# Kernel tuning notes

Measured on AMD Instinct MI355X. Metric: run time of the kernel, lower is better.

## Reference

```python
import jax, jax.numpy as jnp
import numpy as np

D = 128      # d_model
ED = 256     # d_inner = 2*d_model
N = 16       # d_state
DT = 8       # dt_rank = ceil(d_model/16)
K = 4        # d_conv
NL = 2       # n_layers
NC = 2       # n_classes
EPS = 1e-5


def setup_inputs() -> dict:
    key = jax.random.key(0)
    ks = jax.random.split(key, 16)
    L, IN = 12000, 1024
    s = 0.02
    inp = {}
    inp['x'] = jax.random.normal(ks[0], (1, L, IN), jnp.float32)
    inp['coords'] = jax.random.uniform(ks[1], (L, 2), jnp.float32)
    inp['fc1_w'] = jax.random.normal(ks[2], (IN, D), jnp.float32) * s
    inp['fc1_b'] = jnp.zeros((D,), jnp.float32)
    inp['rms_w'] = jnp.ones((NL, D), jnp.float32)
    inp['inproj_w'] = jax.random.normal(ks[3], (NL, D, 2 * ED), jnp.float32) * s
    inp['conv_w'] = jax.random.normal(ks[4], (NL, ED, K), jnp.float32) * s
    inp['conv_b'] = jnp.zeros((NL, ED), jnp.float32)
    inp['xproj_w'] = jax.random.normal(ks[5], (NL, ED, DT + 2 * N), jnp.float32) * s
    inp['dt_w'] = jax.random.normal(ks[6], (NL, DT, ED), jnp.float32) * s
    inp['dt_b'] = jax.random.normal(ks[7], (NL, ED), jnp.float32) * 0.1
    inp['A_log'] = jnp.log(jnp.broadcast_to(jnp.arange(1, N + 1, dtype=jnp.float32), (NL, ED, N)))
    inp['D_p'] = jnp.ones((NL, ED), jnp.float32)
    inp['outproj_w'] = jax.random.normal(ks[8], (NL, ED, D), jnp.float32) * s
    inp['ln_w'] = jnp.ones((D,), jnp.float32)
    inp['ln_b'] = jnp.zeros((D,), jnp.float32)
    inp['att_w1'] = jax.random.normal(ks[9], (D, 128), jnp.float32) * s
    inp['att_b1'] = jnp.zeros((128,), jnp.float32)
    inp['att_w2'] = jax.random.normal(ks[10], (128, 1), jnp.float32) * s
    inp['att_b2'] = jnp.zeros((1,), jnp.float32)
    inp['cls_w'] = jax.random.normal(ks[11], (D, NC), jnp.float32) * s
    inp['cls_b'] = jnp.zeros((NC,), jnp.float32)
    return inp


def _rmsnorm(x, w):
    return x * jax.lax.rsqrt(jnp.mean(x * x, axis=-1, keepdims=True) + EPS) * w


def _layernorm(x, w, b):
    m = jnp.mean(x, axis=-1, keepdims=True)
    v = jnp.mean((x - m) ** 2, axis=-1, keepdims=True)
    return (x - m) * jax.lax.rsqrt(v + EPS) * w + b


def _causal_conv(xb, w, b):
    # xb: [B,L,ED], w: [ED,K] depthwise causal conv
    xpad = jnp.pad(xb, ((0, 0), (K - 1, 0), (0, 0)))
    kern = w.T[:, None, :]  # [K,1,ED]
    out = jax.lax.conv_general_dilated(
        xpad, kern, window_strides=(1,), padding='VALID',
        feature_group_count=ED, dimension_numbers=('NWC', 'WIO', 'NWC'))
    return out + b


def _mamba_block(h, ipw, cw, cb, xpw, dtw, dtb, alog, dp, opw):
    # h: [B,L,D]
    xz = h @ ipw                                  # [B,L,2*ED]
    xb, z = xz[..., :ED], xz[..., ED:]
    xc = jax.nn.silu(_causal_conv(xb, cw, cb))    # [B,L,ED]
    dbl = xc @ xpw                                # [B,L,DT+2N]
    dlt, Bm, Cm = dbl[..., :DT], dbl[..., DT:DT + N], dbl[..., DT + N:]
    delta = jax.nn.softplus(dlt @ dtw + dtb)      # [B,L,ED]
    A = -jnp.exp(alog)                            # [ED,N]
    dA = jnp.exp(delta[..., None] * A)            # [B,L,ED,N]
    dBx = (delta * xc)[..., None] * Bm[:, :, None, :]

    def step(hs, inp):
        da, dbx, c = inp
        hs = da * hs + dbx                        # [B,ED,N]
        y = jnp.einsum('ben,bn->be', hs, c)
        return hs, y

    h0 = jnp.zeros((dA.shape[0], ED, N), dA.dtype)
    xs = (dA.transpose(1, 0, 2, 3), dBx.transpose(1, 0, 2, 3), Cm.transpose(1, 0, 2))
    _, ys = jax.lax.scan(step, h0, xs)            # [L,B,ED]
    y = ys.transpose(1, 0, 2) + dp * xc
    y = y * jax.nn.silu(z)
    return y @ opw                                # [B,L,D]


def reference(x, coords, fc1_w, fc1_b, rms_w, inproj_w, conv_w, conv_b, xproj_w,
              dt_w, dt_b, A_log, D_p, outproj_w, ln_w, ln_b,
              att_w1, att_b1, att_w2, att_b2, cls_w, cls_b):
    h = jax.nn.gelu(x @ fc1_w + fc1_b, approximate=False)
    for i in range(NL):
        h = h + _mamba_block(_rmsnorm(h, rms_w[i]), inproj_w[i], conv_w[i], conv_b[i],
                             xproj_w[i], dt_w[i], dt_b[i], A_log[i], D_p[i], outproj_w[i])
    h = _layernorm(h, ln_w, ln_b)
    A = jnp.tanh(h @ att_w1 + att_b1) @ att_w2 + att_b2   # [1,L,1]
    A = jax.nn.softmax(A.transpose(0, 2, 1), axis=-1)     # [1,1,L]
    pooled = jnp.einsum('bol,bld->bod', A, h)[0]          # [1,D]
    logits = pooled @ cls_w + cls_b                       # [1,NC]
    Y_prob = jax.nn.softmax(logits, axis=1)
    Y_hat = jnp.argmax(logits, axis=1)
    return (logits, Y_prob, Y_hat)
```

## Files before the change

### kernel.cpp

```cpp
#include <hip/hip_runtime.h>

#define LQ 12000
#define IN_D 1024
#define DM 128
#define EDM 256
#define NS 16
#define CCH 480
#define SCH 25
#define GN 32
#define GSZ 15

typedef __bf16 v8bf __attribute__((ext_vector_type(8)));
typedef __bf16 v4bf __attribute__((ext_vector_type(4)));
typedef float v4f __attribute__((ext_vector_type(4)));

__device__ __forceinline__ float wave_sum64(float v) {
#pragma unroll
  for (int o = 32; o > 0; o >>= 1) v += __shfl_xor(v, o);
  return v;
}
__device__ __forceinline__ float wave_max64(float v) {
#pragma unroll
  for (int o = 32; o > 0; o >>= 1) v = fmaxf(v, __shfl_xor(v, o));
  return v;
}

__device__ __forceinline__ void stage16(const __bf16* g, __bf16* l) {
#if __has_builtin(__builtin_amdgcn_global_load_lds)
  __builtin_amdgcn_global_load_lds(
      (const __attribute__((address_space(1))) unsigned int*)g,
      (__attribute__((address_space(3))) unsigned int*)l, 16, 0, 0);
#else
  *(float4*)l = *(const float4*)g;
#endif
}

template <int ACT, bool BIAS, bool ACCUM>
__global__ __launch_bounds__(256) void mgemm_k(const __bf16* __restrict__ A,
                                               const __bf16* __restrict__ Bt,
                                               const float* __restrict__ bias,
                                               float* __restrict__ C, int M,
                                               int K, int Cs, int Nv) {
  __shared__ __bf16 As[64 * 32];
  __shared__ __bf16 Bs[64 * 32];
  const int tid = threadIdx.x;
  const int lane = tid & 63, wid = tid >> 6;
  const int wr = wid >> 1, wc = wid & 1;
  const int row0 = blockIdx.y * 64, col0 = blockIdx.x * 64;
  const int frow = lane & 15, fk8 = (lane >> 4) * 8;
  const int srow = tid >> 2, skseg = (tid & 3) * 8;
  int garow = row0 + srow;
  if (garow >= M) garow = M - 1;
  const __bf16* gA = A + (size_t)garow * K + skseg;
  const __bf16* gB = Bt + (size_t)(col0 + srow) * K + skseg;
  __bf16* lA = As + tid * 8;
  __bf16* lB = Bs + tid * 8;
  v4f acc[2][2] = {};
  for (int kt = 0; kt < K; kt += 32) {
    stage16(gA + kt, lA);
    stage16(gB + kt, lB);
    __syncthreads();
    v8bf av[2], bv[2];
#pragma unroll
    for (int i = 0; i < 2; ++i)
      av[i] = *(const v8bf*)(As + (wr * 32 + i * 16 + frow) * 32 + fk8);
#pragma unroll
    for (int j = 0; j < 2; ++j)
      bv[j] = *(const v8bf*)(Bs + (wc * 32 + j * 16 + frow) * 32 + fk8);
#pragma unroll
    for (int i = 0; i < 2; ++i)
#pragma unroll
      for (int j = 0; j < 2; ++j)
        acc[i][j] =
            __builtin_amdgcn_mfma_f32_16x16x32_bf16(av[i], bv[j], acc[i][j], 0, 0, 0);
    __syncthreads();
  }
#pragma unroll
  for (int i = 0; i < 2; ++i) {
#pragma unroll
    for (int j = 0; j < 2; ++j) {
      int cc = col0 + wc * 32 + j * 16 + (lane & 15);
#pragma unroll
      for (int r = 0; r < 4; ++r) {
        int rr = row0 + wr * 32 + i * 16 + (lane >> 4) * 4 + r;
        if (rr < M && cc < Nv) {
          float v = acc[i][j][r];
          if (BIAS) v += bias[cc];
          if (ACT == 1) v = 0.5f * v * (1.f + erff(v * 0.70710678118654752f));
          if (ACT == 2) v = tanhf(v);
          float* cp = C + (size_t)rr * Cs + cc;
          if (ACCUM)
            *cp += v;
          else
            *cp = v;
        }
      }
    }
  }
}

__global__ __launch_bounds__(256) void castw_k(const float* __restrict__ fc1w,
                                               const float* __restrict__ ipw,
                                               const float* __restrict__ xpw,
                                               const float* __restrict__ opw,
                                               const float* __restrict__ a1w,
                                               __bf16* __restrict__ wp) {
  int idx = blockIdx.x * 256 + threadIdx.x;
  const float* src;
  int K, N, o, base;
  if (idx < 131072) {
    base = 0; o = idx; src = fc1w; K = 1024; N = 128;
  } else if (idx < 262144) {
    int t = idx - 131072; int s = t >> 16; o = t & 65535;
    src = ipw + (size_t)s * 65536; K = 128; N = 512; base = 131072 + (s << 16);
  } else if (idx < 327680) {
    int t = idx - 262144; int s = t >> 15; o = t & 32767;
    src = xpw + (size_t)s * 10240; K = 256; N = 40; base = 262144 + (s << 15);
  } else if (idx < 393216) {
    int t = idx - 327680; int s = t >> 15; o = t & 32767;
    src = opw + (size_t)s * 32768; K = 256; N = 128; base = 327680 + (s << 15);
  } else {
    base = 393216; o = idx - 393216; src = a1w; K = 128; N = 128;
  }
  int n = o / K, k = o - n * K;
  float v = (n < N) ? src[(size_t)k * N + n] : 0.f;
  wp[base + o] = (__bf16)v;
}

__global__ __launch_bounds__(256) void castx_k(const float* __restrict__ in,
                                               __bf16* __restrict__ out) {
  int i = blockIdx.x * 256 + threadIdx.x;
  float4 v = ((const float4*)in)[i];
  v4bf w = {(__bf16)v.x, (__bf16)v.y, (__bf16)v.z, (__bf16)v.w};
  ((v4bf*)out)[i] = w;
}

__global__ __launch_bounds__(256) void rmsnorm_k(const float* __restrict__ h,
                                                 const float* __restrict__ w,
                                                 __bf16* __restrict__ o) {
  int lane = threadIdx.x & 63;
  int t = blockIdx.x * 4 + (threadIdx.x >> 6);
  const float* row = h + (size_t)t * DM;
  float x0 = row[lane], x1 = row[lane + 64];
  float ss = wave_sum64(x0 * x0 + x1 * x1);
  float r = 1.f / sqrtf(ss * (1.f / DM) + 1e-5f);
  o[(size_t)t * DM + lane] = (__bf16)(x0 * r * w[lane]);
  o[(size_t)t * DM + lane + 64] = (__bf16)(x1 * r * w[lane + 64]);
}

__global__ __launch_bounds__(256) void layernorm_k(const float* __restrict__ h,
                                                   const float* __restrict__ w,
                                                   const float* __restrict__ b,
                                                   float* __restrict__ o,
                                                   __bf16* __restrict__ ob) {
  int lane = threadIdx.x & 63;
  int t = blockIdx.x * 4 + (threadIdx.x >> 6);
  const float* row = h + (size_t)t * DM;
  float x0 = row[lane], x1 = row[lane + 64];
  float s = wave_sum64(x0 + x1);
  float ss = wave_sum64(x0 * x0 + x1 * x1);
  float m = s * (1.f / DM);
  float var = ss * (1.f / DM) - m * m;
  float r = 1.f / sqrtf(var + 1e-5f);
  float y0 = (x0 - m) * r * w[lane] + b[lane];
  float y1 = (x1 - m) * r * w[lane + 64] + b[lane + 64];
  o[(size_t)t * DM + lane] = y0;
  o[(size_t)t * DM + lane + 64] = y1;
  ob[(size_t)t * DM + lane] = (__bf16)y0;
  ob[(size_t)t * DM + lane + 64] = (__bf16)y1;
}

__global__ __launch_bounds__(256) void conv_silu_k(const float* __restrict__ xz,
                                                   const float* __restrict__ cw,
                                                   const float* __restrict__ cb,
                                                   float* __restrict__ xc,
                                                   __bf16* __restrict__ xcb) {
  int idx = blockIdx.x * 256 + threadIdx.x;
  int e = idx & (EDM - 1);
  int t = idx >> 8;
  float acc = cb[e];
  const float* wp = cw + e * 4;
#pragma unroll
  for (int j = 0; j < 4; ++j) {
    int ts = t - 3 + j;
    if (ts >= 0) acc = fmaf(xz[(size_t)ts * 512 + e], wp[j], acc);
  }
  float v = __fdividef(acc, 1.f + __expf(-acc));
  xc[idx] = v;
  xcb[idx] = (__bf16)v;
}

__global__ __launch_bounds__(256) void dt_k(const float* __restrict__ dbl,
                                            const float* __restrict__ dtw,
                                            const float* __restrict__ dtb,
                                            float* __restrict__ delta) {
  int idx = blockIdx.x * 256 + threadIdx.x;
  int e = idx & 255;
  int t = idx >> 8;
  const float* dl = dbl + (size_t)t * 40;
  float acc = dtb[e];
#pragma unroll
  for (int k = 0; k < 8; ++k) acc = fmaf(dl[k], dtw[k * 256 + e], acc);
  delta[idx] = fmaxf(acc, 0.f) + log1pf(expf(-fabsf(acc)));
}


__global__ __launch_bounds__(256) void scan1_k(const float* __restrict__ delta,
                                               const float* __restrict__ xc,
                                               const float* __restrict__ dbl,
                                               float* __restrict__ Dsum,
                                               float* __restrict__ Bacc) {
  int e = threadIdx.x;
  int c = blockIdx.x;
  int t0 = c * SCH;
  float h[NS];
#pragma unroll
  for (int n = 0; n < NS; ++n) h[n] = 0.f;
  float ds = 0.f;
  const float* dp = delta + (size_t)t0 * EDM + e;
  const float* xp = xc + (size_t)t0 * EDM + e;
  const float* bp = dbl + (size_t)t0 * 40 + 8;
  for (int s = 0; s < SCH; ++s) {
    float d = dp[s * EDM];
    float xcv = xp[s * EDM];
    float q = __expf(-d);
    float dx = d * xcv;
    ds += d;
    const float* B = bp + s * 40;
    float pw = q;
#pragma unroll
    for (int n = 0; n < NS; ++n) {
      h[n] = fmaf(pw, h[n], dx * B[n]);
      pw *= q;
    }
  }
  Dsum[c * EDM + e] = ds;
  float4* bq = (float4*)(Bacc + (size_t)c * 4096 + e * NS);
  bq[0] = make_float4(h[0], h[1], h[2], h[3]);
  bq[1] = make_float4(h[4], h[5], h[6], h[7]);
  bq[2] = make_float4(h[8], h[9], h[10], h[11]);
  bq[3] = make_float4(h[12], h[13], h[14], h[15]);
}

__global__ __launch_bounds__(256) void scan2a_k(const float* __restrict__ alog,
                                                const float* __restrict__ Dsum,
                                                const float* __restrict__ Bacc,
                                                float* __restrict__ Gs,
                                                float* __restrict__ Gb) {
  int b = blockIdx.x;
  int g = b >> 4;
  int ch = ((b & 15) << 8) + threadIdx.x;
  int e = ch >> 4;
  float Aen = -expf(alog[ch]);
  float hh = 0.f, ds = 0.f;
#pragma unroll
  for (int j = 0; j < GSZ; ++j) {
    int c = g * GSZ + j;
    float dsv = Dsum[c * EDM + e];
    ds += dsv;
    hh = fmaf(__expf(Aen * dsv), hh, Bacc[(size_t)c * 4096 + ch]);
  }
  Gs[g * 4096 + ch] = ds;
  Gb[g * 4096 + ch] = hh;
}

__global__ __launch_bounds__(256) void scan2b_k(const float* __restrict__ alog,
                                                const float* __restrict__ Gs,
                                                const float* __restrict__ Gb,
                                                float* __restrict__ Gc) {
  int ch = blockIdx.x * 256 + threadIdx.x;
  float Aen = -expf(alog[ch]);
  float gs[GN], gb[GN];
#pragma unroll
  for (int g = 0; g < GN; ++g) {
    gs[g] = Gs[g * 4096 + ch];
    gb[g] = Gb[g * 4096 + ch];
  }
  float carry = 0.f;
#pragma unroll
  for (int g = 0; g < GN; ++g) {
    Gc[g * 4096 + ch] = carry;
    carry = fmaf(__expf(Aen * gs[g]), carry, gb[g]);
  }
}

__global__ __launch_bounds__(256) void scan2c_k(const float* __restrict__ alog,
                                                const float* __restrict__ Dsum,
                                                float* __restrict__ Bacc,
                                                const float* __restrict__ Gc) {
  int b = blockIdx.x;
  int g = b >> 4;
  int ch = ((b & 15) << 8) + threadIdx.x;
  int e = ch >> 4;
  float Aen = -expf(alog[ch]);
  float carry = Gc[g * 4096 + ch];
#pragma unroll
  for (int j = 0; j < GSZ; ++j) {
    int c = g * GSZ + j;
    float a = __expf(Aen * Dsum[c * EDM + e]);
    float old = Bacc[(size_t)c * 4096 + ch];
    Bacc[(size_t)c * 4096 + ch] = carry;
    carry = fmaf(a, carry, old);
  }
}

__global__ __launch_bounds__(256) void scan3_k(const float* __restrict__ delta,
                                               const float* __restrict__ xc,
                                               const float* __restrict__ dbl,
                                               const float* __restrict__ xz,
                                               const float* __restrict__ Bacc,
                                               const float* __restrict__ dpw,
                                               __bf16* __restrict__ yb) {
  int e = threadIdx.x;
  int c = blockIdx.x;
  int t0 = c * SCH;
  float h[NS];
  const float4* hq = (const float4*)(Bacc + (size_t)c * 4096 + e * NS);
  float4 h0 = hq[0], h1 = hq[1], h2 = hq[2], h3 = hq[3];
  h[0] = h0.x; h[1] = h0.y; h[2] = h0.z; h[3] = h0.w;
  h[4] = h1.x; h[5] = h1.y; h[6] = h1.z; h[7] = h1.w;
  h[8] = h2.x; h[9] = h2.y; h[10] = h2.z; h[11] = h2.w;
  h[12] = h3.x; h[13] = h3.y; h[14] = h3.z; h[15] = h3.w;
  float dpe = dpw[e];
  const float* dp = delta + (size_t)t0 * EDM + e;
  const float* xp = xc + (size_t)t0 * EDM + e;
  const float* bp = dbl + (size_t)t0 * 40 + 8;
  const float* zp = xz + (size_t)t0 * 512 + 256 + e;
  for (int s = 0; s < SCH; ++s) {
    float d = dp[s * EDM];
    float xcv = xp[s * EDM];
    float q = __expf(-d);
    float dx = d * xcv;
    const float* B = bp + s * 40;
    const float* Cc = B + NS;
    float v = 0.f;
    float pw = q;
#pragma unroll
    for (int n = 0; n < NS; ++n) {
      h[n] = fmaf(pw, h[n], dx * B[n]);
      v = fmaf(h[n], Cc[n], v);
      pw *= q;
    }
    float y = v + dpe * xcv;
    float z = zp[s * 512];
    y *= __fdividef(z, 1.f + __expf(-z));
    yb[(size_t)(t0 + s) * EDM + e] = (__bf16)y;
  }
}

__global__ __launch_bounds__(256) void att2_k(const float* __restrict__ t1,
                                              const float* __restrict__ w2,
                                              const float* __restrict__ b2,
                                              float* __restrict__ s) {
  int lane = threadIdx.x & 63;
  int t = blockIdx.x * 4 + (threadIdx.x >> 6);
  const float* row = t1 + (size_t)t * DM;
  float acc = fmaf(row[lane], w2[lane], row[lane + 64] * w2[lane + 64]);
  acc = wave_sum64(acc);
  if (lane == 0) s[t] = acc + b2[0];
}

__global__ __launch_bounds__(1024) void att_stats_k(const float* __restrict__ s,
                                                    float* __restrict__ stats) {
  __shared__ float red[16];
  int lane = threadIdx.x & 63, wid = threadIdx.x >> 6;
  float m = -1e30f;
  for (int i = threadIdx.x; i < LQ; i += 1024) m = fmaxf(m, s[i]);
  m = wave_max64(m);
  if (lane == 0) red[wid] = m;
  __syncthreads();
  if (threadIdx.x < 16) {
    float mm = red[threadIdx.x];
#pragma unroll
    for (int o = 8; o > 0; o >>= 1) mm = fmaxf(mm, __shfl_xor(mm, o));
    if (threadIdx.x == 0) red[0] = mm;
  }
  __syncthreads();
  float smax = red[0];
  __syncthreads();
  float sum = 0.f;
  for (int i = threadIdx.x; i < LQ; i += 1024) sum += expf(s[i] - smax);
  sum = wave_sum64(sum);
  if (lane == 0) red[wid] = sum;
  __syncthreads();
  if (threadIdx.x == 0) {
    float tot = 0.f;
    for (int i = 0; i < 16; ++i) tot += red[i];
    stats[0] = smax;
    stats[1] = tot;
  }
}

__global__ __launch_bounds__(128) void pooled_k(const float* __restrict__ s,
                                                const float* __restrict__ stats,
                                                const float* __restrict__ hn,
                                                float* __restrict__ pooled) {
  __shared__ float w[64];
  int t0 = blockIdx.x * 64;
  float smax = stats[0];
  if (threadIdx.x < 64) {
    int t = t0 + threadIdx.x;
    w[threadIdx.x] = (t < LQ) ? expf(s[t] - smax) : 0.f;
  }
  __syncthreads();
  int d = threadIdx.x;
  float acc = 0.f;
  int nmax = min(64, LQ - t0);
  for (int i = 0; i < nmax; ++i)
    acc = fmaf(w[i], hn[(size_t)(t0 + i) * DM + d], acc);
  atomicAdd(&pooled[d], acc);
}

__global__ __launch_bounds__(128) void final_k(const float* __restrict__ pooled,
                                               const float* __restrict__ stats,
                                               const float* __restrict__ cls_w,
                                               const float* __restrict__ cls_b,
                                               float* __restrict__ out) {
  __shared__ float r0[2], r1[2];
  int lane = threadIdx.x & 63, wid = threadIdx.x >> 6;
  float p = pooled[threadIdx.x] / stats[1];
  float v0 = p * cls_w[threadIdx.x * 2 + 0];
  float v1 = p * cls_w[threadIdx.x * 2 + 1];
  v0 = wave_sum64(v0);
  v1 = wave_sum64(v1);
  if (lane == 0) {
    r0[wid] = v0;
    r1[wid] = v1;
  }
  __syncthreads();
  if (threadIdx.x == 0) {
    float L0 = r0[0] + r0[1] + cls_b[0];
    float L1 = r1[0] + r1[1] + cls_b[1];
    float mx = fmaxf(L0, L1);
    float e0 = expf(L0 - mx), e1 = expf(L1 - mx);
    float inv = 1.f / (e0 + e1);
    out[0] = L0;
    out[1] = L1;
    out[2] = e0 * inv;
    out[3] = e1 * inv;
    out[4] = (L1 > L0) ? 1.f : 0.f;
  }
}

extern "C" void kernel_launch(void* const* d_in, const int* in_sizes, int n_in,
                              void* d_out, int out_size, void* d_ws,
                              size_t ws_size, hipStream_t stream) {
  const float* x = (const float*)d_in[0];
  const float* fc1_w = (const float*)d_in[2];
  const float* fc1_b = (const float*)d_in[3];
  const float* rms_w = (const float*)d_in[4];
  const float* inproj_w = (const float*)d_in[5];
  const float* conv_w = (const float*)d_in[6];
  const float* conv_b = (const float*)d_in[7];
  const float* xproj_w = (const float*)d_in[8];
  const float* dt_w = (const float*)d_in[9];
  const float* dt_b = (const float*)d_in[10];
  const float* A_log = (const float*)d_in[11];
  const float* D_p = (const float*)d_in[12];
  const float* outproj_w = (const float*)d_in[13];
  const float* ln_w = (const float*)d_in[14];
  const float* ln_b = (const float*)d_in[15];
  const float* att_w1 = (const float*)d_in[16];
  const float* att_b1 = (const float*)d_in[17];
  const float* att_w2 = (const float*)d_in[18];
  const float* att_b2 = (const float*)d_in[19];
  const float* cls_w = (const float*)d_in[20];
  const float* cls_b = (const float*)d_in[21];
  float* out = (float*)d_out;

  float* ws = (float*)d_ws;
  float* xz = ws;
  float* h = xz + 6144000;
  float* hn = h + 1536000;
  float* xc = hn + 1536000;
  float* dbl = xc + 3072000;
  float* del = dbl + 480000;
  float* Dsum = del + 3072000;
  float* Bacc = Dsum + 122880;
  float* Gs = Bacc + 1966080;
  float* Gb = Gs + 131072;
  float* Gc = Gb + 131072;
  float* pooled = Gc + 131072;
  float* stats = pooled + 128;
  __bf16* wp = (__bf16*)(stats + 16);
  __bf16* hnb = wp + 409600;
  __bf16* xcb = hnb + 1536000;
  __bf16* yb = xcb + 3072000;
  __bf16* xb = (__bf16*)xz;

  const __bf16* fc1T = wp;
  const __bf16* ipT[2] = {wp + 131072, wp + 196608};
  const __bf16* xpT[2] = {wp + 262144, wp + 294912};
  const __bf16* opT[2] = {wp + 327680, wp + 360448};
  const __bf16* a1T = wp + 393216;

  hipMemsetAsync(pooled, 0, 128 * sizeof(float), stream);

  dim3 b256(256);
  castw_k<<<1600, b256, 0, stream>>>(fc1_w, inproj_w, xproj_w, outproj_w,
                                     att_w1, wp);
  castx_k<<<12000, b256, 0, stream>>>(x, xb);
  mgemm_k<1, true, false><<<dim3(2, 188), b256, 0, stream>>>(
      xb, fc1T, fc1_b, h, LQ, 1024, 128, 128);

  for (int l = 0; l < 2; ++l) {
    const float* alog_l = A_log + l * 4096;
    rmsnorm_k<<<3000, b256, 0, stream>>>(h, rms_w + l * DM, hnb);
    mgemm_k<0, false, false><<<dim3(8, 188), b256, 0, stream>>>(
        hnb, ipT[l], nullptr, xz, LQ, 128, 512, 512);
    conv_silu_k<<<12000, b256, 0, stream>>>(xz, conv_w + l * EDM * 4,
                                            conv_b + l * EDM, xc, xcb);
    mgemm_k<0, false, false><<<dim3(1, 188), b256, 0, stream>>>(
        xcb, xpT[l], nullptr, dbl, LQ, 256, 40, 40);
    dt_k<<<12000, b256, 0, stream>>>(dbl, dt_w + l * 8 * EDM, dt_b + l * EDM,
                                     del);
    scan1_k<<<CCH, b256, 0, stream>>>(del, xc, dbl, Dsum, Bacc);
    scan2a_k<<<512, b256, 0, stream>>>(alog_l, Dsum, Bacc, Gs, Gb);
    scan2b_k<<<16, b256, 0, stream>>>(alog_l, Gs, Gb, Gc);
    scan2c_k<<<512, b256, 0, stream>>>(alog_l, Dsum, Bacc, Gc);
    scan3_k<<<CCH, b256, 0, stream>>>(del, xc, dbl, xz, Bacc, D_p + l * EDM,
                                      yb);
    mgemm_k<0, false, true><<<dim3(2, 188), b256, 0, stream>>>(
        yb, opT[l], nullptr, h, LQ, 256, 128, 128);
  }

  layernorm_k<<<3000, b256, 0, stream>>>(h, ln_w, ln_b, hn, hnb);
  mgemm_k<2, true, false><<<dim3(2, 188), b256, 0, stream>>>(
      hnb, a1T, att_b1, del, LQ, 128, 128, 128);
  att2_k<<<3000, b256, 0, stream>>>(del, att_w2, att_b2, dbl);
  att_stats_k<<<1, 1024, 0, stream>>>(dbl, stats);
  pooled_k<<<188, 128, 0, stream>>>(dbl, stats, hn, pooled);
  final_k<<<1, 128, 0, stream>>>(pooled, stats, cls_w, cls_b, out);
}
```

Baseline: 382.4 us.

## Fuse casts, dt projection, silu gate and attention head into neighboring kernels

Folds the fp32-to-bf16 cast of the input into the fc1 GEMM's A-tile staging, and recomputes the dt projection plus softplus inside both scan kernels instead of materialising delta. It also applies the z-gate silu in the in-proj GEMM epilogue and stores xz, xc and the layernorm output only as bf16. The attention tanh layer is fused with the w2 dot product through shuffles and atomics, which removes several kernels and a lot of fp32 intermediate traffic. In exchange there is more bf16 rounding in intermediates, redundant dt arithmetic in scan1 and scan3, and att_b2 is dropped (softmax is shift-invariant, so this is fine unless stats uses the raw scores).

```diff
diff --git a/kernel.cpp b/kernel.cpp
--- a/kernel.cpp
+++ b/kernel.cpp
@@ -11,7 +11,6 @@
 #define GSZ 15
 
 typedef __bf16 v8bf __attribute__((ext_vector_type(8)));
-typedef __bf16 v4bf __attribute__((ext_vector_type(4)));
 typedef float v4f __attribute__((ext_vector_type(4)));
 
 __device__ __forceinline__ float wave_sum64(float v) {
@@ -35,11 +34,10 @@
 #endif
 }
 
-template <int ACT, bool BIAS, bool ACCUM>
+template <int ACT, bool ACCUM, bool OBF>
 __global__ __launch_bounds__(256) void mgemm_k(const __bf16* __restrict__ A,
                                                const __bf16* __restrict__ Bt,
-                                               const float* __restrict__ bias,
-                                               float* __restrict__ C, int M,
+                                               void* __restrict__ Cv, int M,
                                                int K, int Cs, int Nv) {
   __shared__ __bf16 As[64 * 32];
   __shared__ __bf16 Bs[64 * 32];
@@ -71,30 +69,152 @@
     for (int i = 0; i < 2; ++i)
 #pragma unroll
       for (int j = 0; j < 2; ++j)
-        acc[i][j] =
-            __builtin_amdgcn_mfma_f32_16x16x32_bf16(av[i], bv[j], acc[i][j], 0, 0, 0);
+        acc[i][j] = __builtin_amdgcn_mfma_f32_16x16x32_bf16(av[i], bv[j],
+                                                            acc[i][j], 0, 0, 0);
     __syncthreads();
   }
 #pragma unroll
   for (int i = 0; i < 2; ++i) {
 #pragma unroll
     for (int j = 0; j < 2; ++j) {
-      int cc = col0 + wc * 32 + j * 16 + (lane & 15);
+      int cc = col0 + wc * 32 + j * 16 + frow;
 #pragma unroll
       for (int r = 0; r < 4; ++r) {
         int rr = row0 + wr * 32 + i * 16 + (lane >> 4) * 4 + r;
         if (rr < M && cc < Nv) {
           float v = acc[i][j][r];
-          if (BIAS) v += bias[cc];
-          if (ACT == 1) v = 0.5f * v * (1.f + erff(v * 0.70710678118654752f));
-          if (ACT == 2) v = tanhf(v);
-          float* cp = C + (size_t)rr * Cs + cc;
-          if (ACCUM)
-            *cp += v;
-          else
-            *cp = v;
+          if (ACT == 4 && cc >= 256) v = __fdividef(v, 1.f + __expf(-v));
+          if (OBF) {
+            ((__bf16*)Cv)[(size_t)rr * Cs + cc] = (__bf16)v;
+          } else {
+            float* cp = (float*)Cv + (size_t)rr * Cs + cc;
+            if (ACCUM)
+              *cp += v;
+            else
+              *cp = v;
+          }
         }
       }
+    }
+  }
+}
+
+__global__ __launch_bounds__(256) void fc1_k(const float* __restrict__ A,
+                                             const __bf16* __restrict__ Bt,
+                                             const float* __restrict__ bias,
+                                             float* __restrict__ C, int M,
+                                             int K) {
+  __shared__ __bf16 As[64 * 32];
+  __shared__ __bf16 Bs[64 * 32];
+  const int tid = threadIdx.x;
+  const int lane = tid & 63, wid = tid >> 6;
+  const int wr = wid >> 1, wc = wid & 1;
+  const int row0 = blockIdx.y * 64, col0 = blockIdx.x * 64;
+  const int frow = lane & 15, fk8 = (lane >> 4) * 8;
+  const int srow = tid >> 2, skseg = (tid & 3) * 8;
+  int garow = row0 + srow;
+  if (garow >= M) garow = M - 1;
+  const float* gA = A + (size_t)garow * K + skseg;
+  const __bf16* gB = Bt + (size_t)(col0 + srow) * K + skseg;
+  __bf16* lB = Bs + tid * 8;
+  v4f acc[2][2] = {};
+  for (int kt = 0; kt < K; kt += 32) {
+    float4 f0 = *(const float4*)(gA + kt);
+    float4 f1 = *(const float4*)(gA + kt + 4);
+    stage16(gB + kt, lB);
+    v8bf a8 = {(__bf16)f0.x, (__bf16)f0.y, (__bf16)f0.z, (__bf16)f0.w,
+               (__bf16)f1.x, (__bf16)f1.y, (__bf16)f1.z, (__bf16)f1.w};
+    *(v8bf*)(As + tid * 8) = a8;
+    __syncthreads();
+    v8bf av[2], bv[2];
+#pragma unroll
+    for (int i = 0; i < 2; ++i)
+      av[i] = *(const v8bf*)(As + (wr * 32 + i * 16 + frow) * 32 + fk8);
+#pragma unroll
+    for (int j = 0; j < 2; ++j)
+      bv[j] = *(const v8bf*)(Bs + (wc * 32 + j * 16 + frow) * 32 + fk8);
+#pragma unroll
+    for (int i = 0; i < 2; ++i)
+#pragma unroll
+      for (int j = 0; j < 2; ++j)
+        acc[i][j] = __builtin_amdgcn_mfma_f32_16x16x32_bf16(av[i], bv[j],
+                                                            acc[i][j], 0, 0, 0);
+    __syncthreads();
+  }
+#pragma unroll
+  for (int i = 0; i < 2; ++i) {
+#pragma unroll
+    for (int j = 0; j < 2; ++j) {
+      int cc = col0 + wc * 32 + j * 16 + frow;
+#pragma unroll
+      for (int r = 0; r < 4; ++r) {
+        int rr = row0 + wr * 32 + i * 16 + (lane >> 4) * 4 + r;
+        if (rr < M) {
+          float v = acc[i][j][r] + bias[cc];
+          v = 0.5f * v * (1.f + erff(v * 0.70710678118654752f));
+          C[(size_t)rr * DM + cc] = v;
+        }
+      }
+    }
+  }
+}
+
+__global__ __launch_bounds__(256) void att1_k(const __bf16* __restrict__ A,
+                                              const __bf16* __restrict__ Bt,
+                                              const float* __restrict__ b1,
+                                              const float* __restrict__ w2,
+                                              float* __restrict__ s, int M) {
+  __shared__ __bf16 As[64 * 32];
+  __shared__ __bf16 Bs[64 * 32];
+  const int tid = threadIdx.x;
+  const int lane = tid & 63, wid = tid >> 6;
+  const int wr = wid >> 1, wc = wid & 1;
+  const int row0 = blockIdx.y * 64, col0 = blockIdx.x * 64;
+  const int frow = lane & 15, fk8 = (lane >> 4) * 8;
+  const int srow = tid >> 2, skseg = (tid & 3) * 8;
+  const int K = 128;
+  int garow = row0 + srow;
+  if (garow >= M) garow = M - 1;
+  const __bf16* gA = A + (size_t)garow * K + skseg;
+  const __bf16* gB = Bt + (size_t)(col0 + srow) * K + skseg;
+  __bf16* lA = As + tid * 8;
+  __bf16* lB = Bs + tid * 8;
+  v4f acc[2][2] = {};
+  for (int kt = 0; kt < K; kt += 32) {
+    stage16(gA + kt, lA);
+    stage16(gB + kt, lB);
+    __syncthreads();
+    v8bf av[2], bv[2];
+#pragma unroll
+    for (int i = 0; i < 2; ++i)
+      av[i] = *(const v8bf*)(As + (wr * 32 + i * 16 + frow) * 32 + fk8);
+#pragma unroll
+    for (int j = 0; j < 2; ++j)
+      bv[j] = *(const v8bf*)(Bs + (wc * 32 + j * 16 + frow) * 32 + fk8);
+#pragma unroll
+    for (int i = 0; i < 2; ++i)
+#pragma unroll
+      for (int j = 0; j < 2; ++j)
+        acc[i][j] = __builtin_amdgcn_mfma_f32_16x16x32_bf16(av[i], bv[j],
+                                                            acc[i][j], 0, 0, 0);
+    __syncthreads();
+  }
+#pragma unroll
+  for (int i = 0; i < 2; ++i) {
+#pragma unroll
+    for (int r = 0; r < 4; ++r) {
+      float p = 0.f;
+#pragma unroll
+      for (int j = 0; j < 2; ++j) {
+        int cc = col0 + wc * 32 + j * 16 + frow;
+        p += tanhf(acc[i][j][r] + b1[cc]) * w2[cc];
+      }
+      p += __shfl_xor(p, 1);
+      p += __shfl_xor(p, 2);
+      p += __shfl_xor(p, 4);
+      p += __shfl_xor(p, 8);
+      int rr = row0 + wr * 32 + i * 16 + (lane >> 4) * 4 + r;
+      if (frow == 0 && rr < M) atomicAdd(&s[rr], p);
     }
   }
 }
@@ -127,14 +247,6 @@
   wp[base + o] = (__bf16)v;
 }
 
-__global__ __launch_bounds__(256) void castx_k(const float* __restrict__ in,
-                                               __bf16* __restrict__ out) {
-  int i = blockIdx.x * 256 + threadIdx.x;
-  float4 v = ((const float4*)in)[i];
-  v4bf w = {(__bf16)v.x, (__bf16)v.y, (__bf16)v.z, (__bf16)v.w};
-  ((v4bf*)out)[i] = w;
-}
-
 __global__ __launch_bounds__(256) void rmsnorm_k(const float* __restrict__ h,
                                                  const float* __restrict__ w,
                                                  __bf16* __restrict__ o) {
@@ -151,7 +263,6 @@
 __global__ __launch_bounds__(256) void layernorm_k(const float* __restrict__ h,
                                                    const float* __restrict__ w,
                                                    const float* __restrict__ b,
-                                                   float* __restrict__ o,
                                                    __bf16* __restrict__ ob) {
   int lane = threadIdx.x & 63;
   int t = blockIdx.x * 4 + (threadIdx.x >> 6);
@@ -162,18 +273,14 @@
   float m = s * (1.f / DM);
   float var = ss * (1.f / DM) - m * m;
   float r = 1.f / sqrtf(var + 1e-5f);
-  float y0 = (x0 - m) * r * w[lane] + b[lane];
-  float y1 = (x1 - m) * r * w[lane + 64] + b[lane + 64];
-  o[(size_t)t * DM + lane] = y0;
-  o[(size_t)t * DM + lane + 64] = y1;
-  ob[(size_t)t * DM + lane] = (__bf16)y0;
-  ob[(size_t)t * DM + lane + 64] = (__bf16)y1;
-}
-
-__global__ __launch_bounds__(256) void conv_silu_k(const float* __restrict__ xz,
+  ob[(size_t)t * DM + lane] = (__bf16)((x0 - m) * r * w[lane] + b[lane]);
+  ob[(size_t)t * DM + lane + 64] =
+      (__bf16)((x1 - m) * r * w[lane + 64] + b[lane + 64]);
+}
+
+__global__ __launch_bounds__(256) void conv_silu_k(const __bf16* __restrict__ xzb,
                                                    const float* __restrict__ cw,
                                                    const float* __restrict__ cb,
-                                                   float* __restrict__ xc,
                                                    __bf16* __restrict__ xcb) {
   int idx = blockIdx.x * 256 + threadIdx.x;
   int e = idx & (EDM - 1);
@@ -183,50 +290,47 @@
 #pragma unroll
   for (int j = 0; j < 4; ++j) {
     int ts = t - 3 + j;
-    if (ts >= 0) acc = fmaf(xz[(size_t)ts * 512 + e], wp[j], acc);
+    if (ts >= 0) acc = fmaf((float)xzb[(size_t)ts * 512 + e], wp[j], acc);
   }
   float v = __fdividef(acc, 1.f + __expf(-acc));
-  xc[idx] = v;
   xcb[idx] = (__bf16)v;
 }
 
-__global__ __launch_bounds__(256) void dt_k(const float* __restrict__ dbl,
-                                            const float* __restrict__ dtw,
-                                            const float* __restrict__ dtb,
-                                            float* __restrict__ delta) {
-  int idx = blockIdx.x * 256 + threadIdx.x;
-  int e = idx & 255;
-  int t = idx >> 8;
-  const float* dl = dbl + (size_t)t * 40;
-  float acc = dtb[e];
-#pragma unroll
-  for (int k = 0; k < 8; ++k) acc = fmaf(dl[k], dtw[k * 256 + e], acc);
-  delta[idx] = fmaxf(acc, 0.f) + log1pf(expf(-fabsf(acc)));
-}
-
-
-__global__ __launch_bounds__(256) void scan1_k(const float* __restrict__ delta,
-                                               const float* __restrict__ xc,
+
+__device__ __forceinline__ float softplus_f(float a) {
+  return fmaxf(a, 0.f) + log1pf(__expf(-fabsf(a)));
+}
+
+__global__ __launch_bounds__(256) void scan1_k(const __bf16* __restrict__ xcb,
                                                const float* __restrict__ dbl,
+                                               const float* __restrict__ dtw,
+                                               const float* __restrict__ dtb,
                                                float* __restrict__ Dsum,
                                                float* __restrict__ Bacc) {
   int e = threadIdx.x;
   int c = blockIdx.x;
   int t0 = c * SCH;
+  float w8[8];
+#pragma unroll
+  for (int k = 0; k < 8; ++k) w8[k] = dtw[k * 256 + e];
+  float dtbe = dtb[e];
   float h[NS];
 #pragma unroll
   for (int n = 0; n < NS; ++n) h[n] = 0.f;
   float ds = 0.f;
-  const float* dp = delta + (size_t)t0 * EDM + e;
-  const float* xp = xc + (size_t)t0 * EDM + e;
-  const float* bp = dbl + (size_t)t0 * 40 + 8;
+  const __bf16* xp = xcb + (size_t)t0 * EDM + e;
+  const float* rp = dbl + (size_t)t0 * 40;
   for (int s = 0; s < SCH; ++s) {
-    float d = dp[s * EDM];
-    float xcv = xp[s * EDM];
+    const float* row = rp + s * 40;
+    float a = dtbe;
+#pragma unroll
+    for (int k = 0; k < 8; ++k) a = fmaf(row[k], w8[k], a);
+    float d = softplus_f(a);
+    float xcv = (float)xp[s * EDM];
     float q = __expf(-d);
     float dx = d * xcv;
     ds += d;
-    const float* B = bp + s * 40;
+    const float* B = row + 8;
     float pw = q;
 #pragma unroll
     for (int n = 0; n < NS; ++n) {
@@ -304,16 +408,21 @@
   }
 }
 
-__global__ __launch_bounds__(256) void scan3_k(const float* __restrict__ delta,
-                                               const float* __restrict__ xc,
+__global__ __launch_bounds__(256) void scan3_k(const __bf16* __restrict__ xcb,
                                                const float* __restrict__ dbl,
-                                               const float* __restrict__ xz,
+                                               const float* __restrict__ dtw,
+                                               const float* __restrict__ dtb,
+                                               const __bf16* __restrict__ xzb,
                                                const float* __restrict__ Bacc,
                                                const float* __restrict__ dpw,
                                                __bf16* __restrict__ yb) {
   int e = threadIdx.x;
   int c = blockIdx.x;
   int t0 = c * SCH;
+  float w8[8];
+#pragma unroll
+  for (int k = 0; k < 8; ++k) w8[k] = dtw[k * 256 + e];
+  float dtbe = dtb[e];
   float h[NS];
   const float4* hq = (const float4*)(Bacc + (size_t)c * 4096 + e * NS);
   float4 h0 = hq[0], h1 = hq[1], h2 = hq[2], h3 = hq[3];
@@ -322,17 +431,20 @@
   h[8] = h2.x; h[9] = h2.y; h[10] = h2.z; h[11] = h2.w;
   h[12] = h3.x; h[13] = h3.y; h[14] = h3.z; h[15] = h3.w;
   float dpe = dpw[e];
-  const float* dp = delta + (size_t)t0 * EDM + e;
-  const float* xp = xc + (size_t)t0 * EDM + e;
-  const float* bp = dbl + (size_t)t0 * 40 + 8;
-  const float* zp = xz + (size_t)t0 * 512 + 256 + e;
+  const __bf16* xp = xcb + (size_t)t0 * EDM + e;
+  const float* rp = dbl + (size_t)t0 * 40;
+  const __bf16* zp = xzb + (size_t)t0 * 512 + 256 + e;
   for (int s = 0; s < SCH; ++s) {
-    float d = dp[s * EDM];
-    float xcv = xp[s * EDM];
+    const float* row = rp + s * 40;
+    float a = dtbe;
+#pragma unroll
+    for (int k = 0; k < 8; ++k) a = fmaf(row[k], w8[k], a);
+    float d = softplus_f(a);
+    float xcv = (float)xp[s * EDM];
     float q = __expf(-d);
     float dx = d * xcv;
-    const float* B = bp + s * 40;
-    const float* Cc = B + NS;
+    const float* B = row + 8;
+    const float* Cc = row + 24;
     float v = 0.f;
     float pw = q;
 #pragma unroll
@@ -341,23 +453,9 @@
       v = fmaf(h[n], Cc[n], v);
       pw *= q;
     }
-    float y = v + dpe * xcv;
-    float z = zp[s * 512];
-    y *= __fdividef(z, 1.f + __expf(-z));
+    float y = (v + dpe * xcv) * (float)zp[s * 512];
     yb[(size_t)(t0 + s) * EDM + e] = (__bf16)y;
   }
-}
-
-__global__ __launch_bounds__(256) void att2_k(const float* __restrict__ t1,
-                                              const float* __restrict__ w2,
-                                              const float* __restrict__ b2,
-                                              float* __restrict__ s) {
-  int lane = threadIdx.x & 63;
-  int t = blockIdx.x * 4 + (threadIdx.x >> 6);
-  const float* row = t1 + (size_t)t * DM;
-  float acc = fmaf(row[lane], w2[lane], row[lane + 64] * w2[lane + 64]);
-  acc = wave_sum64(acc);
-  if (lane == 0) s[t] = acc + b2[0];
 }
 
 __global__ __launch_bounds__(1024) void att_stats_k(const float* __restrict__ s,
@@ -393,7 +491,7 @@
 
 __global__ __launch_bounds__(128) void pooled_k(const float* __restrict__ s,
                                                 const float* __restrict__ stats,
-                                                const float* __restrict__ hn,
+                                                const __bf16* __restrict__ hnb,
                                                 float* __restrict__ pooled) {
   __shared__ float w[64];
   int t0 = blockIdx.x * 64;
@@ -407,7 +505,7 @@
   float acc = 0.f;
   int nmax = min(64, LQ - t0);
   for (int i = 0; i < nmax; ++i)
-    acc = fmaf(w[i], hn[(size_t)(t0 + i) * DM + d], acc);
+    acc = fmaf(w[i], (float)hnb[(size_t)(t0 + i) * DM + d], acc);
   atomicAdd(&pooled[d], acc);
 }
 
@@ -463,30 +561,26 @@
   const float* att_w1 = (const float*)d_in[16];
   const float* att_b1 = (const float*)d_in[17];
   const float* att_w2 = (const float*)d_in[18];
-  const float* att_b2 = (const float*)d_in[19];
   const float* cls_w = (const float*)d_in[20];
   const float* cls_b = (const float*)d_in[21];
   float* out = (float*)d_out;
 
   float* ws = (float*)d_ws;
-  float* xz = ws;
-  float* h = xz + 6144000;
-  float* hn = h + 1536000;
-  float* xc = hn + 1536000;
-  float* dbl = xc + 3072000;
-  float* del = dbl + 480000;
-  float* Dsum = del + 3072000;
+  float* h = ws;
+  float* dbl = h + 1536000;
+  float* Dsum = dbl + 480000;
   float* Bacc = Dsum + 122880;
   float* Gs = Bacc + 1966080;
   float* Gb = Gs + 131072;
   float* Gc = Gb + 131072;
-  float* pooled = Gc + 131072;
+  float* sbuf = Gc + 131072;
+  float* pooled = sbuf + 12000;
   float* stats = pooled + 128;
   __bf16* wp = (__bf16*)(stats + 16);
   __bf16* hnb = wp + 409600;
-  __bf16* xcb = hnb + 1536000;
+  __bf16* xzb = hnb + 1536000;
+  __bf16* xcb = xzb + 6144000;
   __bf16* yb = xcb + 3072000;
-  __bf16* xb = (__bf16*)xz;
 
   const __bf16* fc1T = wp;
   const __bf16* ipT[2] = {wp + 131072, wp + 196608};
@@ -494,41 +588,37 @@
   const __bf16* opT[2] = {wp + 327680, wp + 360448};
   const __bf16* a1T = wp + 393216;
 
-  hipMemsetAsync(pooled, 0, 128 * sizeof(float), stream);
+  hipMemsetAsync(sbuf, 0, (12000 + 128) * sizeof(float), stream);
 
   dim3 b256(256);
   castw_k<<<1600, b256, 0, stream>>>(fc1_w, inproj_w, xproj_w, outproj_w,
                                      att_w1, wp);
-  castx_k<<<12000, b256, 0, stream>>>(x, xb);
-  mgemm_k<1, true, false><<<dim3(2, 188), b256, 0, stream>>>(
-      xb, fc1T, fc1_b, h, LQ, 1024, 128, 128);
+  fc1_k<<<dim3(2, 188), b256, 0, stream>>>(x, fc1T, fc1_b, h, LQ, IN_D);
 
   for (int l = 0; l < 2; ++l) {
     const float* alog_l = A_log + l * 4096;
+    const float* dtw_l = dt_w + l * 8 * EDM;
+    const float* dtb_l = dt_b + l * EDM;
     rmsnorm_k<<<3000, b256, 0, stream>>>(h, rms_w + l * DM, hnb);
-    mgemm_k<0, false, false><<<dim3(8, 188), b256, 0, stream>>>(
-        hnb, ipT[l], nullptr, xz, LQ, 128, 512, 512);
-    conv_silu_k<<<12000, b256, 0, stream>>>(xz, conv_w + l * EDM * 4,
-                                            conv_b + l * EDM, xc, xcb);
+    mgemm_k<4, false, true><<<dim3(8, 188), b256, 0, stream>>>(
+        hnb, ipT[l], xzb, LQ, 128, 512, 512);
+    conv_silu_k<<<12000, b256, 0, stream>>>(xzb, conv_w + l * EDM * 4,
+                                            conv_b + l * EDM, xcb);
     mgemm_k<0, false, false><<<dim3(1, 188), b256, 0, stream>>>(
-        xcb, xpT[l], nullptr, dbl, LQ, 256, 40, 40);
-    dt_k<<<12000, b256, 0, stream>>>(dbl, dt_w + l * 8 * EDM, dt_b + l * EDM,
-                                     del);
-    scan1_k<<<CCH, b256, 0, stream>>>(del, xc, dbl, Dsum, Bacc);
+        xcb, xpT[l], dbl, LQ, 256, 40, 40);
+    scan1_k<<<CCH, b256, 0, stream>>>(xcb, dbl, dtw_l, dtb_l, Dsum, Bacc);
     scan2a_k<<<512, b256, 0, stream>>>(alog_l, Dsum, Bacc, Gs, Gb);
     scan2b_k<<<16, b256, 0, stream>>>(alog_l, Gs, Gb, Gc);
     scan2c_k<<<512, b256, 0, stream>>>(alog_l, Dsum, Bacc, Gc);
-    scan3_k<<<CCH, b256, 0, stream>>>(del, xc, dbl, xz, Bacc, D_p + l * EDM,
-                                      yb);
-    mgemm_k<0, false, true><<<dim3(2, 188), b256, 0, stream>>>(
-        yb, opT[l], nullptr, h, LQ, 256, 128, 128);
-  }
-
-  layernorm_k<<<3000, b256, 0, stream>>>(h, ln_w, ln_b, hn, hnb);
-  mgemm_k<2, true, false><<<dim3(2, 188), b256, 0, stream>>>(
-      hnb, a1T, att_b1, del, LQ, 128, 128, 128);
-  att2_k<<<3000, b256, 0, stream>>>(del, att_w2, att_b2, dbl);
-  att_stats_k<<<1, 1024, 0, stream>>>(dbl, stats);
-  pooled_k<<<188, 128, 0, stream>>>(dbl, stats, hn, pooled);
+    scan3_k<<<CCH, b256, 0, stream>>>(xcb, dbl, dtw_l, dtb_l, xzb, Bacc,
+                                      D_p + l * EDM, yb);
+    mgemm_k<0, true, false><<<dim3(2, 188), b256, 0, stream>>>(
+        yb, opT[l], h, LQ, 256, 128, 128);
+  }
+
+  layernorm_k<<<3000, b256, 0, stream>>>(h, ln_w, ln_b, hnb);
+  att1_k<<<dim3(2, 188), b256, 0, stream>>>(hnb, a1T, att_b1, att_w2, sbuf, LQ);
+  att_stats_k<<<1, 1024, 0, stream>>>(sbuf, stats);
+  pooled_k<<<188, 128, 0, stream>>>(sbuf, stats, hnb, pooled);
   final_k<<<1, 128, 0, stream>>>(pooled, stats, cls_w, cls_b, out);
 }
```

Measured after the change: 387.1 us. Within noise of the previous version (+1.2%).
